# Kernel optimization log

Measured on AMD Instinct MI355X. Metric: run time of the kernel, lower is better.

Reference implementation:

```python
import jax, jax.numpy as jnp
import numpy as np

N, D, R, OUT, B = 4096, 128, 8, 128, 4096

def setup_inputs() -> dict:
    key = jax.random.key(0)
    ks = jax.random.split(key, 8)
    return {
        "embeddings": jax.random.normal(ks[0], (N, D), dtype=jnp.float32),
        "head_idx": jax.random.randint(ks[1], (B,), 0, N),
        "head_e": jax.random.normal(ks[2], (B, D), dtype=jnp.float32),
        "tail_idx": jax.random.randint(ks[3], (B,), 0, N),
        "tail_e": jax.random.normal(ks[4], (B, D), dtype=jnp.float32),
        "adj_mats": jax.random.uniform(ks[5], (R, N, N), dtype=jnp.float32),
        "relation_kernel": jax.random.normal(ks[6], (R, D, OUT), dtype=jnp.float32),
        "self_kernel": jax.random.normal(ks[7], (D, OUT), dtype=jnp.float32),
    }

def _branch(idx, e, adj_mats, embeddings, relation_kernel, self_kernel):
    # self transform: [B, OUT]
    out = e @ self_kernel
    # per-relation row gather: [R, B, N]
    adj = adj_mats[:, idx, :]
    # neighborhood aggregation: [R, B, D]
    upd = jnp.einsum('rbn,nd->rbd', adj, embeddings)
    # relation transform + accumulate over relations: [B, OUT]
    out = out + jnp.einsum('rbd,rdo->bo', upd, relation_kernel)
    return out

def reference(embeddings, head_idx, head_e, tail_idx, tail_e, adj_mats, relation_kernel, self_kernel):
    head_output = _branch(head_idx, head_e, adj_mats, embeddings, relation_kernel, self_kernel)
    tail_output = _branch(tail_idx, tail_e, adj_mats, embeddings, relation_kernel, self_kernel)
    return (head_output, tail_output)
```

## Files before the change

### kernel.cpp

```cpp
#include <hip/hip_runtime.h>

#define NN   4096
#define DD   128
#define RR   8
#define OUTD 128
#define BB   4096

typedef unsigned short ushort_t;
typedef __attribute__((ext_vector_type(8))) short short8;
typedef __attribute__((ext_vector_type(4))) float floatx4;

__device__ __forceinline__ ushort_t f2bf(float f) {
  union { float f; unsigned int u; } v; v.f = f;
  unsigned int u = v.u;
  return (ushort_t)((u + 0x7fffu + ((u >> 16) & 1u)) >> 16);
}

__device__ __forceinline__ unsigned int pk2(float x, float y) {
  union { float f; unsigned int u; } a, b;
  a.f = x; b.f = y;
  const unsigned int ua = a.u + 0x8000u;
  const unsigned int ub = b.u + 0x8000u;
  return __builtin_amdgcn_perm(ub, ua, 0x07060302u);
}

__device__ __forceinline__ short8 pack8(float4 a, float4 b) {
  union { unsigned int u[4]; short8 s; } r;
  r.u[0] = pk2(a.x, a.y); r.u[1] = pk2(a.z, a.w);
  r.u[2] = pk2(b.x, b.y); r.u[3] = pk2(b.z, b.w);
  return r.s;
}

__global__ __launch_bounds__(256) void compute_wt(const float* __restrict__ emb,
                                                  const float* __restrict__ rk,
                                                  ushort_t* __restrict__ Wt) {
  __shared__ float e_s[64][132];
  __shared__ float k_s[128][36];
  const int r  = blockIdx.y;
  const int m0 = blockIdx.x * 64;
  const int t  = threadIdx.x;
  {
    const int row = t >> 2, q = t & 3;
    const float* src = emb + (size_t)(m0 + row) * DD;
    #pragma unroll
    for (int j = 0; j < 8; ++j) {
      const int c = q + 4 * j;
      *(float4*)&e_s[row][c * 4] = *(const float4*)(src + c * 4);
    }
  }
  const int m_l = t >> 2, ob = (t & 3) * 8;
  const float* rkr = rk + (size_t)r * DD * OUTD;
  #pragma unroll 1
  for (int oc = 0; oc < 4; ++oc) {
    __syncthreads();
    {
      const int d = t >> 1, h = (t & 1) * 4;
      #pragma unroll
      for (int j = 0; j < 4; ++j) {
        const int c = h + j;
        *(float4*)&k_s[d][c * 4] = *(const float4*)(rkr + d * OUTD + oc * 32 + c * 4);
      }
    }
    __syncthreads();
    float acc[8] = {0, 0, 0, 0, 0, 0, 0, 0};
    #pragma unroll 4
    for (int d = 0; d < DD; ++d) {
      const float e  = e_s[m_l][d];
      const float4 w0 = *(const float4*)&k_s[d][ob];
      const float4 w1 = *(const float4*)&k_s[d][ob + 4];
      acc[0] += e * w0.x; acc[1] += e * w0.y; acc[2] += e * w0.z; acc[3] += e * w0.w;
      acc[4] += e * w1.x; acc[5] += e * w1.y; acc[6] += e * w1.z; acc[7] += e * w1.w;
    }
    ushort_t* dst = Wt + ((size_t)r * OUTD + oc * 32 + ob) * NN + m0 + m_l;
    #pragma unroll
    for (int j = 0; j < 8; ++j) dst[(size_t)j * NN] = f2bf(acc[j]);
  }
}

__global__ __launch_bounds__(256) void rgcn_main(const float* __restrict__ adj,
                                                 const ushort_t* __restrict__ Wt,
                                                 float* __restrict__ Z) {
  __shared__ short8 A8[1024];
  __shared__ short8 B8[2048];
  const int r     = blockIdx.y >> 1;
  const int khalf = (blockIdx.y & 1) * 2048;
  const int n0    = blockIdx.x * 64;
  const int t = threadIdx.x;
  const int lane = t & 63, wave = t >> 6;
  const int wm = wave >> 1, wn = wave & 1;
  const int l15 = lane & 15, l4 = lane >> 4;
  const float*    adjr = adj + (size_t)r * NN * NN + (size_t)n0 * NN;
  const ushort_t* wtr  = Wt + (size_t)r * OUTD * NN;

  floatx4 acc[2][4] = {};

  const int arow = t >> 2, aq = t & 3;

  for (int k0 = khalf; k0 < khalf + 2048; k0 += 128) {
    const float4* asrc = (const float4*)(adjr + (size_t)arow * NN + k0) + aq * 8;
    float4 av[8];
    #pragma unroll
    for (int j = 0; j < 8; ++j) av[j] = asrc[j];
    #pragma unroll
    for (int it = 0; it < 8; ++it) {
      const int s = wave * 512 + it * 64 + lane;
      const int o = s >> 4, kc = s & 15;
      const int gkc = kc ^ (o & 15);
      const ushort_t* gp = wtr + (size_t)o * NN + k0 + gkc * 8;
      __builtin_amdgcn_global_load_lds(
          (const __attribute__((address_space(1))) void*)gp,
          (__attribute__((address_space(3))) void*)&B8[wave * 512 + it * 64],
          16, 0, 0);
    }
    #pragma unroll
    for (int j = 0; j < 4; ++j) {
      const int ck = aq * 4 + j;
      A8[arow * 16 + (ck ^ (arow & 15))] = pack8(av[2 * j], av[2 * j + 1]);
    }
    __syncthreads();
    #pragma unroll
    for (int kk = 0; kk < 4; ++kk) {
      short8 af[2], bf[4];
      #pragma unroll
      for (int ti = 0; ti < 2; ++ti) {
        const int row = wm * 32 + ti * 16 + l15;
        af[ti] = A8[row * 16 + ((kk * 4 + l4) ^ (row & 15))];
      }
      #pragma unroll
      for (int tj = 0; tj < 4; ++tj) {
        const int orow = wn * 64 + tj * 16 + l15;
        bf[tj] = B8[orow * 16 + ((kk * 4 + l4) ^ (orow & 15))];
      }
      #pragma unroll
      for (int ti = 0; ti < 2; ++ti)
        #pragma unroll
        for (int tj = 0; tj < 4; ++tj)
          acc[ti][tj] = __builtin_amdgcn_mfma_f32_16x16x32_bf16(af[ti], bf[tj],
                                                                acc[ti][tj], 0, 0, 0);
    }
    __syncthreads();
  }
  #pragma unroll
  for (int ti = 0; ti < 2; ++ti)
    #pragma unroll
    for (int tj = 0; tj < 4; ++tj)
      #pragma unroll
      for (int j = 0; j < 4; ++j) {
        const int nrow = n0 + wm * 32 + ti * 16 + l4 * 4 + j;
        const int ocol = wn * 64 + tj * 16 + l15;
        atomicAdd(Z + (size_t)nrow * OUTD + ocol, acc[ti][tj][j]);
      }
}

__global__ __launch_bounds__(256) void epilogue_k(const float* __restrict__ he,
                                                  const float* __restrict__ te,
                                                  const int* __restrict__ hidx,
                                                  const int* __restrict__ tidx,
                                                  const float* __restrict__ sk,
                                                  const float* __restrict__ Z,
                                                  float* __restrict__ out) {
  __shared__ float e_s[64][132];
  __shared__ float k_s[128][36];
  const int bx = blockIdx.x;
  const int branch = bx >> 6;
  const int row0 = (bx & 63) * 64;
  const float* e  = branch ? te : he;
  const int* idx  = branch ? tidx : hidx;
  float* ob = out + (size_t)branch * BB * OUTD;
  const int t = threadIdx.x;
  {
    const int row = t >> 2, q = t & 3;
    const float* src = e + (size_t)(row0 + row) * DD;
    #pragma unroll
    for (int j = 0; j < 8; ++j) {
      const int c = q + 4 * j;
      *(float4*)&e_s[row][c * 4] = *(const float4*)(src + c * 4);
    }
  }
  const int m_l = t >> 2, obk = (t & 3) * 8;
  const int zi = idx[row0 + m_l];
  const float* zrow = Z + (size_t)zi * OUTD;
  #pragma unroll 1
  for (int oc = 0; oc < 4; ++oc) {
    __syncthreads();
    {
      const int d = t >> 1, h = (t & 1) * 4;
      #pragma unroll
      for (int j = 0; j < 4; ++j) {
        const int c = h + j;
        *(float4*)&k_s[d][c * 4] = *(const float4*)(sk + d * OUTD + oc * 32 + c * 4);
      }
    }
    __syncthreads();
    float acc[8] = {0, 0, 0, 0, 0, 0, 0, 0};
    #pragma unroll 4
    for (int d = 0; d < DD; ++d) {
      const float ev = e_s[m_l][d];
      const float4 w0 = *(const float4*)&k_s[d][obk];
      const float4 w1 = *(const float4*)&k_s[d][obk + 4];
      acc[0] += ev * w0.x; acc[1] += ev * w0.y; acc[2] += ev * w0.z; acc[3] += ev * w0.w;
      acc[4] += ev * w1.x; acc[5] += ev * w1.y; acc[6] += ev * w1.z; acc[7] += ev * w1.w;
    }
    const float4 z0 = *(const float4*)(zrow + oc * 32 + obk);
    const float4 z1 = *(const float4*)(zrow + oc * 32 + obk + 4);
    float4 o0, o1;
    o0.x = acc[0] + z0.x; o0.y = acc[1] + z0.y; o0.z = acc[2] + z0.z; o0.w = acc[3] + z0.w;
    o1.x = acc[4] + z1.x; o1.y = acc[5] + z1.y; o1.z = acc[6] + z1.z; o1.w = acc[7] + z1.w;
    *(float4*)&ob[(size_t)(row0 + m_l) * OUTD + oc * 32 + obk]     = o0;
    *(float4*)&ob[(size_t)(row0 + m_l) * OUTD + oc * 32 + obk + 4] = o1;
  }
}

extern "C" void kernel_launch(void* const* d_in, const int* in_sizes, int n_in,
                              void* d_out, int out_size, void* d_ws, size_t ws_size,
                              hipStream_t stream) {
  const float* emb  = (const float*)d_in[0];
  const int*   hidx = (const int*)  d_in[1];
  const float* he   = (const float*)d_in[2];
  const int*   tidx = (const int*)  d_in[3];
  const float* te   = (const float*)d_in[4];
  const float* adj  = (const float*)d_in[5];
  const float* rk   = (const float*)d_in[6];
  const float* sk   = (const float*)d_in[7];
  float* out = (float*)d_out;

  ushort_t* Wt = (ushort_t*)d_ws;
  float*    Z  = (float*)((char*)d_ws + (size_t)RR * OUTD * NN * sizeof(ushort_t));

  hipMemsetAsync(Z, 0, (size_t)NN * OUTD * sizeof(float), stream);
  compute_wt<<<dim3(64, 8), 256, 0, stream>>>(emb, rk, Wt);
  rgcn_main<<<dim3(64, 16), 256, 0, stream>>>(adj, Wt, Z);
  epilogue_k<<<dim3(128), 256, 0, stream>>>(he, te, hidx, tidx, sk, Z, out);
}
```

Measured before the change: 756.2 us.

## Drop LDS staging in RGCN main GEMM and fuse Z zeroing into compute_wt

The main adjacency×W kernel no longer stages tiles in shared memory. Each wave now owns 16 rows and all 128 output columns, loads A and B fragments straight from global memory into registers, and double-buffers them one 32-wide k-step ahead. This removes the barriers and LDS round trips. The separate memset of Z is folded into the compute_wt kernel. The cost is that Wt is fetched separately by every wave, so it relies more on cache. Adjacency reads also become narrower per-row segments, which may hurt coalescing.

After: 934.0 us. 23.5% more time.

```diff
diff --git a/kernel.cpp b/kernel.cpp
--- a/kernel.cpp
+++ b/kernel.cpp
@@ -33,12 +33,19 @@
 
 __global__ __launch_bounds__(256) void compute_wt(const float* __restrict__ emb,
                                                   const float* __restrict__ rk,
-                                                  ushort_t* __restrict__ Wt) {
+                                                  ushort_t* __restrict__ Wt,
+                                                  float* __restrict__ Z) {
   __shared__ float e_s[64][132];
   __shared__ float k_s[128][36];
   const int r  = blockIdx.y;
   const int m0 = blockIdx.x * 64;
   const int t  = threadIdx.x;
+  if (r == 0) {
+    float4 zv = {0.f, 0.f, 0.f, 0.f};
+    float4* zp = (float4*)Z + (size_t)blockIdx.x * 2048 + t;
+    #pragma unroll
+    for (int j = 0; j < 8; ++j) zp[j * 256] = zv;
+  }
   {
     const int row = t >> 2, q = t & 3;
     const float* src = emb + (size_t)(m0 + row) * DD;
@@ -77,79 +84,56 @@
   }
 }
 
-__global__ __launch_bounds__(256) void rgcn_main(const float* __restrict__ adj,
-                                                 const ushort_t* __restrict__ Wt,
-                                                 float* __restrict__ Z) {
-  __shared__ short8 A8[1024];
-  __shared__ short8 B8[2048];
+__global__ __launch_bounds__(256, 3) void rgcn_main(const float* __restrict__ adj,
+                                                    const ushort_t* __restrict__ Wt,
+                                                    float* __restrict__ Z) {
   const int r     = blockIdx.y >> 1;
   const int khalf = (blockIdx.y & 1) * 2048;
-  const int n0    = blockIdx.x * 64;
-  const int t = threadIdx.x;
-  const int lane = t & 63, wave = t >> 6;
-  const int wm = wave >> 1, wn = wave & 1;
-  const int l15 = lane & 15, l4 = lane >> 4;
-  const float*    adjr = adj + (size_t)r * NN * NN + (size_t)n0 * NN;
-  const ushort_t* wtr  = Wt + (size_t)r * OUTD * NN;
-
-  floatx4 acc[2][4] = {};
-
-  const int arow = t >> 2, aq = t & 3;
-
-  for (int k0 = khalf; k0 < khalf + 2048; k0 += 128) {
-    const float4* asrc = (const float4*)(adjr + (size_t)arow * NN + k0) + aq * 8;
-    float4 av[8];
-    #pragma unroll
-    for (int j = 0; j < 8; ++j) av[j] = asrc[j];
-    #pragma unroll
-    for (int it = 0; it < 8; ++it) {
-      const int s = wave * 512 + it * 64 + lane;
-      const int o = s >> 4, kc = s & 15;
-      const int gkc = kc ^ (o & 15);
-      const ushort_t* gp = wtr + (size_t)o * NN + k0 + gkc * 8;
-      __builtin_amdgcn_global_load_lds(
-          (const __attribute__((address_space(1))) void*)gp,
-          (__attribute__((address_space(3))) void*)&B8[wave * 512 + it * 64],
-          16, 0, 0);
-    }
+  const int t     = threadIdx.x;
+  const int lane  = t & 63, wave = t >> 6;
+  const int l15 = lane & 15, q = lane >> 4;
+  const int m0  = blockIdx.x * 64 + wave * 16;
+
+  const float*    arow = adj + (size_t)r * NN * NN + (size_t)(m0 + l15) * NN + q * 8;
+  const ushort_t* brow = Wt + (size_t)r * OUTD * NN + (size_t)l15 * NN + q * 8;
+
+  floatx4 acc[8] = {};
+
+  short8 aF, bF[8];
+  {
+    const float4* ap = (const float4*)(arow + khalf);
+    float4 a0 = ap[0], a1 = ap[1];
+    #pragma unroll
+    for (int tj = 0; tj < 8; ++tj)
+      bF[tj] = *(const short8*)(brow + (size_t)tj * 16 * NN + khalf);
+    aF = pack8(a0, a1);
+  }
+
+  #pragma unroll 2
+  for (int k0 = khalf; k0 < khalf + 2048; k0 += 32) {
+    const int kn = (k0 + 32 < khalf + 2048) ? (k0 + 32) : khalf;
+    const float4* ap = (const float4*)(arow + kn);
+    float4 a0 = ap[0], a1 = ap[1];
+    short8 bN[8];
+    #pragma unroll
+    for (int tj = 0; tj < 8; ++tj)
+      bN[tj] = *(const short8*)(brow + (size_t)tj * 16 * NN + kn);
+    #pragma unroll
+    for (int tj = 0; tj < 8; ++tj)
+      acc[tj] = __builtin_amdgcn_mfma_f32_16x16x32_bf16(aF, bF[tj], acc[tj], 0, 0, 0);
+    aF = pack8(a0, a1);
+    #pragma unroll
+    for (int tj = 0; tj < 8; ++tj) bF[tj] = bN[tj];
+  }
+
+  #pragma unroll
+  for (int tj = 0; tj < 8; ++tj)
     #pragma unroll
     for (int j = 0; j < 4; ++j) {
-      const int ck = aq * 4 + j;
-      A8[arow * 16 + (ck ^ (arow & 15))] = pack8(av[2 * j], av[2 * j + 1]);
-    }
-    __syncthreads();
-    #pragma unroll
-    for (int kk = 0; kk < 4; ++kk) {
-      short8 af[2], bf[4];
-      #pragma unroll
-      for (int ti = 0; ti < 2; ++ti) {
-        const int row = wm * 32 + ti * 16 + l15;
-        af[ti] = A8[row * 16 + ((kk * 4 + l4) ^ (row & 15))];
-      }
-      #pragma unroll
-      for (int tj = 0; tj < 4; ++tj) {
-        const int orow = wn * 64 + tj * 16 + l15;
-        bf[tj] = B8[orow * 16 + ((kk * 4 + l4) ^ (orow & 15))];
-      }
-      #pragma unroll
-      for (int ti = 0; ti < 2; ++ti)
-        #pragma unroll
-        for (int tj = 0; tj < 4; ++tj)
-          acc[ti][tj] = __builtin_amdgcn_mfma_f32_16x16x32_bf16(af[ti], bf[tj],
-                                                                acc[ti][tj], 0, 0, 0);
-    }
-    __syncthreads();
-  }
-  #pragma unroll
-  for (int ti = 0; ti < 2; ++ti)
-    #pragma unroll
-    for (int tj = 0; tj < 4; ++tj)
-      #pragma unroll
-      for (int j = 0; j < 4; ++j) {
-        const int nrow = n0 + wm * 32 + ti * 16 + l4 * 4 + j;
-        const int ocol = wn * 64 + tj * 16 + l15;
-        atomicAdd(Z + (size_t)nrow * OUTD + ocol, acc[ti][tj][j]);
-      }
+      const int nrow = m0 + q * 4 + j;
+      const int ocol = tj * 16 + l15;
+      atomicAdd(Z + (size_t)nrow * OUTD + ocol, acc[tj][j]);
+    }
 }
 
 __global__ __launch_bounds__(256) void epilogue_k(const float* __restrict__ he,
@@ -227,8 +211,7 @@
   ushort_t* Wt = (ushort_t*)d_ws;
   float*    Z  = (float*)((char*)d_ws + (size_t)RR * OUTD * NN * sizeof(ushort_t));
 
-  hipMemsetAsync(Z, 0, (size_t)NN * OUTD * sizeof(float), stream);
-  compute_wt<<<dim3(64, 8), 256, 0, stream>>>(emb, rk, Wt);
+  compute_wt<<<dim3(64, 8), 256, 0, stream>>>(emb, rk, Wt, Z);
   rgcn_main<<<dim3(64, 16), 256, 0, stream>>>(adj, Wt, Z);
   epilogue_k<<<dim3(128), 256, 0, stream>>>(he, te, hidx, tidx, sk, Z, out);
 }
```
